# Kernel tuning notes

Hardware: AMD Instinct MI355X
Metric: run time of the kernel (lower is better)

Reference implementation:

```python
import jax, jax.numpy as jnp
import numpy as np

FWD_TRUNCATION = 0.05
EPS_LOG = 1e-20


def setup_inputs() -> dict:
    key = jax.random.key(0)
    k1, k2, k3, k4, k5 = jax.random.split(key, 5)
    B, N, M = 32768, 1024, 64
    samples = jax.random.normal(k1, (B, M), dtype=jnp.float32)
    mask = jax.random.uniform(k2, (B, M), dtype=jnp.float32)
    centroids = jax.random.normal(k3, (N, M), dtype=jnp.float32)
    # sd kept away from 0 to avoid huge 1/sd scaling
    sd = jax.random.uniform(k4, (1, M), dtype=jnp.float32) + 0.5
    log_marginal = jax.random.normal(k5, (1, N), dtype=jnp.float32)
    return {"samples": samples, "mask": mask, "centroids": centroids,
            "sd": sd, "log_marginal": log_marginal}


def _masked_pairwise_sq_distances(A, B, mask):
    # A: [B, M] samples, B: [N, M] centroids, mask: [B, M]
    sq_mask = mask * mask
    mA = mask * A
    A_d = jnp.sum(mA * mA, axis=1, keepdims=True)            # [B, 1]
    B_d = sq_mask @ (B * B).T                                 # [B, N]
    cross = (sq_mask * A) @ B.T                                # [B, N]
    return jax.nn.relu(A_d - 2.0 * cross + B_d)               # [B, N]


def _pdf_truncate(pdf, truncation):
    # discretePdfTruncate: zero out entries below truncation * rowmax, renormalize
    threshold = truncation * jnp.max(pdf, axis=-1, keepdims=True)
    pdf = jax.nn.relu(jnp.sign(pdf - threshold)) * pdf
    return pdf / jnp.sum(pdf, axis=-1, keepdims=True)


def reference(samples, mask, centroids, sd, log_marginal):
    # Mahalanobis: fold 1/sd into the mask (sqMahalanobisDistances)
    m = mask / sd
    dist = _masked_pairwise_sq_distances(samples, centroids, m)  # [B, N]
    log_prior = jax.nn.log_softmax(log_marginal, axis=-1)        # [1, N]
    logits = log_prior - 0.5 * dist                              # [B, N]
    # softmaxWithTemperature (temperature=1) -> truncate -> renormalize
    pdf = jax.nn.softmax(logits, axis=-1)
    pdf = _pdf_truncate(pdf, FWD_TRUNCATION)
    log_pdf = jnp.log(pdf + EPS_LOG)                             # logPdfTruncate
    return pdf, log_pdf
```

## Files before the change

kernel.cpp:

```cpp
#include <hip/hip_runtime.h>
#include <math.h>

#define N_C 1024
#define M_F 64
#define B_R 32768
#define R_B 32
#define LDX 132

typedef short bf16x8 __attribute__((ext_vector_type(8)));
typedef float f32x4 __attribute__((ext_vector_type(4)));
typedef unsigned int uint4v __attribute__((ext_vector_type(4)));

__device__ __forceinline__ short f2bf(float x) {
  unsigned b = __float_as_uint(x);
  b += 0x7fffu + ((b >> 16) & 1u);
  return (short)(b >> 16);
}
__device__ __forceinline__ float bf2f(short h) {
  return __uint_as_float(((unsigned)(unsigned short)h) << 16);
}

__device__ __forceinline__ void split3(const float* f, bf16x8& h, bf16x8& m, bf16x8& l) {
  uint4v hp, mp, lp;
#pragma unroll
  for (int i = 0; i < 4; ++i) {
    const unsigned b0 = __float_as_uint(f[2 * i]);
    const unsigned b1 = __float_as_uint(f[2 * i + 1]);
    const unsigned h0 = b0 & 0xFFFF0000u, h1 = b1 & 0xFFFF0000u;
    const float r0 = f[2 * i] - __uint_as_float(h0);
    const float r1 = f[2 * i + 1] - __uint_as_float(h1);
    hp[i] = (b0 >> 16) | h1;
    const unsigned rb0 = __float_as_uint(r0), rb1 = __float_as_uint(r1);
    const unsigned m0 = rb0 & 0xFFFF0000u, m1 = rb1 & 0xFFFF0000u;
    const float s0 = r0 - __uint_as_float(m0);
    const float s1 = r1 - __uint_as_float(m1);
    mp[i] = (rb0 >> 16) | m1;
    lp[i] = (__float_as_uint(s0) >> 16) | (__float_as_uint(s1) & 0xFFFF0000u);
  }
  h = __builtin_bit_cast(bf16x8, hp);
  m = __builtin_bit_cast(bf16x8, mp);
  l = __builtin_bit_cast(bf16x8, lp);
}

__global__ void prep(const float* __restrict__ centroids,
                     const float* __restrict__ lm,
                     bf16x8* __restrict__ yh, bf16x8* __restrict__ ym,
                     bf16x8* __restrict__ yl, float* __restrict__ lp) {
  __shared__ float red[256];
  const int t = threadIdx.x;

  if (blockIdx.x == 64) {
    float v[4];
    float mx = -INFINITY;
#pragma unroll
    for (int i = 0; i < 4; ++i) { v[i] = lm[i * 256 + t]; mx = fmaxf(mx, v[i]); }
    red[t] = mx;
    __syncthreads();
    for (int s = 128; s > 0; s >>= 1) {
      if (t < s) red[t] = fmaxf(red[t], red[t + s]);
      __syncthreads();
    }
    mx = red[0];
    __syncthreads();
    float sum = 0.f;
#pragma unroll
    for (int i = 0; i < 4; ++i) { v[i] -= mx; sum += expf(v[i]); }
    red[t] = sum;
    __syncthreads();
    for (int s = 128; s > 0; s >>= 1) {
      if (t < s) red[t] += red[t + s];
      __syncthreads();
    }
    const float l = logf(red[0]);
#pragma unroll
    for (int i = 0; i < 4; ++i) lp[i * 256 + t] = v[i] - l;
    return;
  }

  const int tid = blockIdx.x * 256 + t;
  const int l = tid & 63;
  const int c = (tid >> 6) & 63;
  const int s = tid >> 12;
  const int n = c * 16 + (l & 15);
  const int k0 = s * 32 + (l >> 4) * 8;
  bf16x8 h, mid, lo;
#pragma unroll
  for (int j = 0; j < 8; ++j) {
    const int k = k0 + j;
    float y;
    if (k < 64) {
      y = centroids[n * M_F + k];
    } else {
      const float cc = centroids[n * M_F + (k - 64)];
      y = cc * cc;
    }
    const short hh = f2bf(y);
    const float r1 = y - bf2f(hh);
    const short mm = f2bf(r1);
    const float r2 = r1 - bf2f(mm);
    h[j] = hh;
    mid[j] = mm;
    lo[j] = f2bf(r2);
  }
  const int blob = (s * 64 + c) * 64 + l;
  yh[blob] = h;
  ym[blob] = mid;
  yl[blob] = lo;
}

__global__ __launch_bounds__(256, 2) void rmm_main(
    const float* __restrict__ samples, const float* __restrict__ mask,
    const float* __restrict__ sd, const float* __restrict__ lp_g,
    const bf16x8* __restrict__ yh_g, const bf16x8* __restrict__ ym_g,
    const bf16x8* __restrict__ yl_g, float* __restrict__ out) {
  __shared__ float xs[R_B * LDX];
  __shared__ float lp_s[N_C];
  __shared__ float ad_s[R_B];
  __shared__ float red_s[R_B * 4];

  const int t = threadIdx.x;
  const int b0 = blockIdx.x * R_B;
  const int w = t >> 6;
  const int l = t & 63;
  const int m = l & 15;
  const int q = l >> 4;

  *(float4*)(lp_s + (t << 2)) = *(const float4*)(lp_g + (t << 2));

  const size_t base0 = (size_t)(w * 16) * 64 + l;
  bf16x8 Bh[2][2], Bm[2][2], Bl[2][2];
#pragma unroll
  for (int p = 0; p < 2; ++p)
#pragma unroll
    for (int e = 0; e < 2; ++e) {
      Bh[p][e] = yh_g[base0 + (p * 2 + e) * 64];
      Bm[p][e] = ym_g[base0 + (p * 2 + e) * 64];
      Bl[p][e] = yl_g[base0 + (p * 2 + e) * 64];
    }

  {
    const int r = t >> 3;
    const int j8 = (t & 7) << 3;
    const float* sp = samples + (size_t)(b0 + r) * M_F + j8;
    const float* mp = mask + (size_t)(b0 + r) * M_F + j8;
    float sa[8], ma[8], da[8];
    *(float4*)&sa[0] = *(const float4*)sp;
    *(float4*)&sa[4] = *(const float4*)(sp + 4);
    *(float4*)&ma[0] = *(const float4*)mp;
    *(float4*)&ma[4] = *(const float4*)(mp + 4);
    *(float4*)&da[0] = *(const float4*)(sd + j8);
    *(float4*)&da[4] = *(const float4*)(sd + j8 + 4);
    float ad = 0.f;
#pragma unroll
    for (int k = 0; k < 8; ++k) {
      const float mm = ma[k] / da[k];
      const float uu = mm * mm;
      const float mA = mm * sa[k];
      ad = fmaf(mA, mA, ad);
      xs[r * LDX + j8 + k] = -2.0f * (uu * sa[k]);
      xs[r * LDX + 64 + j8 + k] = uu;
    }
#pragma unroll
    for (int off = 1; off < 8; off <<= 1) ad += __shfl_xor(ad, off, 64);
    if ((t & 7) == 0) ad_s[r] = ad;
  }

  f32x4 acc[2][16];
#pragma unroll
  for (int mt = 0; mt < 2; ++mt)
#pragma unroll
    for (int c = 0; c < 16; ++c) acc[mt][c] = (f32x4){0.f, 0.f, 0.f, 0.f};

  __syncthreads();

  const int sx[8] = {1, 2, 0, 1, 2, 0, 1, 0};
  const int sy[8] = {2, 1, 2, 1, 0, 1, 0, 0};

#pragma unroll 1
  for (int s = 0; s < 4; ++s) {
    const size_t sbase = (size_t)(s * 64 + w * 16) * 64 + l;
    const bf16x8* yh = yh_g + sbase;
    const bf16x8* ym = ym_g + sbase;
    const bf16x8* yl = yl_g + sbase;

    bf16x8 A[3][2];
#pragma unroll
    for (int mt = 0; mt < 2; ++mt) {
      const float* xp = &xs[(mt * 16 + m) * LDX + s * 32 + q * 8];
      float av[8];
      *(float4*)&av[0] = *(const float4*)xp;
      *(float4*)&av[4] = *(const float4*)(xp + 4);
      split3(av, A[0][mt], A[1][mt], A[2][mt]);
    }

#pragma unroll
    for (int cp = 0; cp < 8; ++cp) {
      const int buf = cp & 1;
      const bf16x8 bh0 = Bh[buf][0], bm0 = Bm[buf][0], bl0 = Bl[buf][0];
      const bf16x8 bh1 = Bh[buf][1], bm1 = Bm[buf][1], bl1 = Bl[buf][1];
      const int pf0 = 2 * cp + 4;
      if (s < 3 || pf0 + 1 < 16) {
        const int o0 = (pf0 < 16) ? pf0 * 64 : 4096 + (pf0 - 16) * 64;
        const int o1 = (pf0 + 1 < 16) ? (pf0 + 1) * 64 : 4096 + (pf0 - 15) * 64;
        Bh[buf][0] = yh[o0]; Bm[buf][0] = ym[o0]; Bl[buf][0] = yl[o0];
        Bh[buf][1] = yh[o1]; Bm[buf][1] = ym[o1]; Bl[buf][1] = yl[o1];
      }
      const int c0 = 2 * cp, c1 = 2 * cp + 1;
#pragma unroll
      for (int sp = 0; sp < 8; ++sp) {
        const bf16x8 b0 = (sy[sp] == 0) ? bh0 : ((sy[sp] == 1) ? bm0 : bl0);
        const bf16x8 b1 = (sy[sp] == 0) ? bh1 : ((sy[sp] == 1) ? bm1 : bl1);
#pragma unroll
        for (int mt = 0; mt < 2; ++mt)
          acc[mt][c0] = __builtin_amdgcn_mfma_f32_16x16x32_bf16(
              A[sx[sp]][mt], b0, acc[mt][c0], 0, 0, 0);
#pragma unroll
        for (int mt = 0; mt < 2; ++mt)
          acc[mt][c1] = __builtin_amdgcn_mfma_f32_16x16x32_bf16(
              A[sx[sp]][mt], b1, acc[mt][c1], 0, 0, 0);
      }
    }
  }

  float adv[2][4];
#pragma unroll
  for (int mt = 0; mt < 2; ++mt)
#pragma unroll
    for (int g = 0; g < 4; ++g) adv[mt][g] = ad_s[mt * 16 + q * 4 + g];
  float lpv[16];
#pragma unroll
  for (int c = 0; c < 16; ++c) lpv[c] = lp_s[w * 256 + c * 16 + m];

#pragma unroll
  for (int mt = 0; mt < 2; ++mt)
#pragma unroll
    for (int c = 0; c < 16; ++c)
#pragma unroll
      for (int g = 0; g < 4; ++g) {
        const float dist = fmaxf(adv[mt][g] + acc[mt][c][g], 0.0f);
        acc[mt][c][g] = lpv[c] - 0.5f * dist;
      }

  float mx[2][4];
#pragma unroll
  for (int mt = 0; mt < 2; ++mt)
#pragma unroll
    for (int g = 0; g < 4; ++g) {
      float v = acc[mt][0][g];
#pragma unroll
      for (int c = 1; c < 16; ++c) v = fmaxf(v, acc[mt][c][g]);
#pragma unroll
      for (int off = 1; off < 16; off <<= 1) v = fmaxf(v, __shfl_xor(v, off, 64));
      mx[mt][g] = v;
    }
  if (m == 0) {
#pragma unroll
    for (int mt = 0; mt < 2; ++mt)
#pragma unroll
      for (int g = 0; g < 4; ++g) red_s[(mt * 16 + q * 4 + g) * 4 + w] = mx[mt][g];
  }
  __syncthreads();
#pragma unroll
  for (int mt = 0; mt < 2; ++mt)
#pragma unroll
    for (int g = 0; g < 4; ++g) {
      const float4 rv = *(const float4*)(&red_s[(mt * 16 + q * 4 + g) * 4]);
      mx[mt][g] = fmaxf(fmaxf(rv.x, rv.y), fmaxf(rv.z, rv.w));
    }
  __syncthreads();

  float sm[2][4];
#pragma unroll
  for (int mt = 0; mt < 2; ++mt)
#pragma unroll
    for (int g = 0; g < 4; ++g) {
      float ssum = 0.f;
#pragma unroll
      for (int c = 0; c < 16; ++c) {
        const float e = __expf(acc[mt][c][g] - mx[mt][g]);
        acc[mt][c][g] = e;
        ssum += e;
      }
#pragma unroll
      for (int off = 1; off < 16; off <<= 1) ssum += __shfl_xor(ssum, off, 64);
      sm[mt][g] = ssum;
    }
  if (m == 0) {
#pragma unroll
    for (int mt = 0; mt < 2; ++mt)
#pragma unroll
      for (int g = 0; g < 4; ++g) red_s[(mt * 16 + q * 4 + g) * 4 + w] = sm[mt][g];
  }
  __syncthreads();
#pragma unroll
  for (int mt = 0; mt < 2; ++mt)
#pragma unroll
    for (int g = 0; g < 4; ++g) {
      const float4 rv = *(const float4*)(&red_s[(mt * 16 + q * 4 + g) * 4]);
      sm[mt][g] = (rv.x + rv.y) + (rv.z + rv.w);
    }
  __syncthreads();

  float thr[2][4], qs[2][4];
#pragma unroll
  for (int mt = 0; mt < 2; ++mt)
#pragma unroll
    for (int g = 0; g < 4; ++g) {
      const float S1 = sm[mt][g];
      thr[mt][g] = 0.05f * (1.0f / S1);
      float s2 = 0.f;
#pragma unroll
      for (int c = 0; c < 16; ++c) {
        const float p = acc[mt][c][g] / S1;
        acc[mt][c][g] = p;
        s2 += (p > thr[mt][g]) ? p : 0.0f;
      }
#pragma unroll
      for (int off = 1; off < 16; off <<= 1) s2 += __shfl_xor(s2, off, 64);
      qs[mt][g] = s2;
    }
  if (m == 0) {
#pragma unroll
    for (int mt = 0; mt < 2; ++mt)
#pragma unroll
      for (int g = 0; g < 4; ++g) red_s[(mt * 16 + q * 4 + g) * 4 + w] = qs[mt][g];
  }
  __syncthreads();
#pragma unroll
  for (int mt = 0; mt < 2; ++mt)
#pragma unroll
    for (int g = 0; g < 4; ++g) {
      const float4 rv = *(const float4*)(&red_s[(mt * 16 + q * 4 + g) * 4]);
      qs[mt][g] = (rv.x + rv.y) + (rv.z + rv.w);
    }

  const size_t colbase = (size_t)(w * 256 + m);
#pragma unroll
  for (int mt = 0; mt < 2; ++mt)
#pragma unroll
    for (int g = 0; g < 4; ++g) {
      const float rq = 1.0f / qs[mt][g];
      float* orow = out + (size_t)(b0 + mt * 16 + q * 4 + g) * N_C + colbase;
      float* lrow = orow + (size_t)B_R * N_C;
#pragma unroll
      for (int c = 0; c < 16; ++c) {
        const float p = acc[mt][c][g];
        const float pf = (p > thr[mt][g]) ? (p * rq) : 0.0f;
        orow[c * 16] = pf;
        lrow[c * 16] = __logf(pf + 1e-20f);
      }
    }
}

extern "C" void kernel_launch(void* const* d_in, const int* in_sizes, int n_in,
                              void* d_out, int out_size, void* d_ws, size_t ws_size,
                              hipStream_t stream) {
  const float* samples   = (const float*)d_in[0];
  const float* mask      = (const float*)d_in[1];
  const float* centroids = (const float*)d_in[2];
  const float* sd        = (const float*)d_in[3];
  const float* lm        = (const float*)d_in[4];
  float* out = (float*)d_out;

  char* ws = (char*)d_ws;
  float* lp  = (float*)ws;
  bf16x8* yh = (bf16x8*)(ws + 4096);
  bf16x8* ym = (bf16x8*)(ws + 4096 + 262144);
  bf16x8* yl = (bf16x8*)(ws + 4096 + 2 * 262144);

  prep<<<65, 256, 0, stream>>>(centroids, lm, yh, ym, yl, lp);
  rmm_main<<<B_R / R_B, 256, 0, stream>>>(samples, mask, sd, lp, yh, ym, yl, out);
}
```

Measured before the change: 334.5 us.

## Process two row tiles per block with double-buffered sample staging

The grid is halved so each block handles two 32-row tiles. The second tile's sample/mask preprocessing is issued before the first tile's epilogue, and the B-fragment prefetch is refilled during that epilogue, so loads overlap compute. The log is also skipped for truncated entries, which now receive a precomputed log(1e-20) constant. This doubles the LDS used for the x buffers, which may lower occupancy, and leaves fewer blocks to spread across the CUs.

```diff
diff --git a/kernel.cpp b/kernel.cpp
--- a/kernel.cpp
+++ b/kernel.cpp
@@ -6,6 +6,7 @@
 #define B_R 32768
 #define R_B 32
 #define LDX 132
+#define NBLK 512
 
 typedef short bf16x8 __attribute__((ext_vector_type(8)));
 typedef float f32x4 __attribute__((ext_vector_type(4)));
@@ -108,74 +109,44 @@
   yl[blob] = lo;
 }
 
-__global__ __launch_bounds__(256, 2) void rmm_main(
-    const float* __restrict__ samples, const float* __restrict__ mask,
-    const float* __restrict__ sd, const float* __restrict__ lp_g,
-    const bf16x8* __restrict__ yh_g, const bf16x8* __restrict__ ym_g,
-    const bf16x8* __restrict__ yl_g, float* __restrict__ out) {
-  __shared__ float xs[R_B * LDX];
-  __shared__ float lp_s[N_C];
-  __shared__ float ad_s[R_B];
-  __shared__ float red_s[R_B * 4];
-
-  const int t = threadIdx.x;
-  const int b0 = blockIdx.x * R_B;
-  const int w = t >> 6;
-  const int l = t & 63;
-  const int m = l & 15;
-  const int q = l >> 4;
-
-  *(float4*)(lp_s + (t << 2)) = *(const float4*)(lp_g + (t << 2));
-
-  const size_t base0 = (size_t)(w * 16) * 64 + l;
-  bf16x8 Bh[2][2], Bm[2][2], Bl[2][2];
-#pragma unroll
-  for (int p = 0; p < 2; ++p)
-#pragma unroll
-    for (int e = 0; e < 2; ++e) {
-      Bh[p][e] = yh_g[base0 + (p * 2 + e) * 64];
-      Bm[p][e] = ym_g[base0 + (p * 2 + e) * 64];
-      Bl[p][e] = yl_g[base0 + (p * 2 + e) * 64];
-    }
-
-  {
-    const int r = t >> 3;
-    const int j8 = (t & 7) << 3;
-    const float* sp = samples + (size_t)(b0 + r) * M_F + j8;
-    const float* mp = mask + (size_t)(b0 + r) * M_F + j8;
-    float sa[8], ma[8], da[8];
-    *(float4*)&sa[0] = *(const float4*)sp;
-    *(float4*)&sa[4] = *(const float4*)(sp + 4);
-    *(float4*)&ma[0] = *(const float4*)mp;
-    *(float4*)&ma[4] = *(const float4*)(mp + 4);
-    *(float4*)&da[0] = *(const float4*)(sd + j8);
-    *(float4*)&da[4] = *(const float4*)(sd + j8 + 4);
-    float ad = 0.f;
-#pragma unroll
-    for (int k = 0; k < 8; ++k) {
-      const float mm = ma[k] / da[k];
-      const float uu = mm * mm;
-      const float mA = mm * sa[k];
-      ad = fmaf(mA, mA, ad);
-      xs[r * LDX + j8 + k] = -2.0f * (uu * sa[k]);
-      xs[r * LDX + 64 + j8 + k] = uu;
-    }
-#pragma unroll
-    for (int off = 1; off < 8; off <<= 1) ad += __shfl_xor(ad, off, 64);
-    if ((t & 7) == 0) ad_s[r] = ad;
-  }
-
-  f32x4 acc[2][16];
-#pragma unroll
-  for (int mt = 0; mt < 2; ++mt)
-#pragma unroll
-    for (int c = 0; c < 16; ++c) acc[mt][c] = (f32x4){0.f, 0.f, 0.f, 0.f};
-
-  __syncthreads();
-
+__device__ __forceinline__ void xbuild(const float* __restrict__ samples,
+                                       const float* __restrict__ mask,
+                                       const float* __restrict__ sd,
+                                       int b0, int t, float* xsb, float* adb) {
+  const int r = t >> 3;
+  const int j8 = (t & 7) << 3;
+  const float* sp = samples + (size_t)(b0 + r) * M_F + j8;
+  const float* mp = mask + (size_t)(b0 + r) * M_F + j8;
+  float sa[8], ma[8], da[8];
+  *(float4*)&sa[0] = *(const float4*)sp;
+  *(float4*)&sa[4] = *(const float4*)(sp + 4);
+  *(float4*)&ma[0] = *(const float4*)mp;
+  *(float4*)&ma[4] = *(const float4*)(mp + 4);
+  *(float4*)&da[0] = *(const float4*)(sd + j8);
+  *(float4*)&da[4] = *(const float4*)(sd + j8 + 4);
+  float ad = 0.f;
+#pragma unroll
+  for (int k = 0; k < 8; ++k) {
+    const float mm = ma[k] / da[k];
+    const float uu = mm * mm;
+    const float mA = mm * sa[k];
+    ad = fmaf(mA, mA, ad);
+    xsb[r * LDX + j8 + k] = -2.0f * (uu * sa[k]);
+    xsb[r * LDX + 64 + j8 + k] = uu;
+  }
+#pragma unroll
+  for (int off = 1; off < 8; off <<= 1) ad += __shfl_xor(ad, off, 64);
+  if ((t & 7) == 0) adb[r] = ad;
+}
+
+__device__ __forceinline__ void kloop(const bf16x8* __restrict__ yh_g,
+                                      const bf16x8* __restrict__ ym_g,
+                                      const bf16x8* __restrict__ yl_g,
+                                      const float* xsb, int w, int l, int m, int q,
+                                      bf16x8 (&Bh)[2][2], bf16x8 (&Bm)[2][2],
+                                      bf16x8 (&Bl)[2][2], f32x4 (&acc)[2][16]) {
   const int sx[8] = {1, 2, 0, 1, 2, 0, 1, 0};
   const int sy[8] = {2, 1, 2, 1, 0, 1, 0, 0};
-
 #pragma unroll 1
   for (int s = 0; s < 4; ++s) {
     const size_t sbase = (size_t)(s * 64 + w * 16) * 64 + l;
@@ -186,7 +157,7 @@
     bf16x8 A[3][2];
 #pragma unroll
     for (int mt = 0; mt < 2; ++mt) {
-      const float* xp = &xs[(mt * 16 + m) * LDX + s * 32 + q * 8];
+      const float* xp = &xsb[(mt * 16 + m) * LDX + s * 32 + q * 8];
       float av[8];
       *(float4*)&av[0] = *(const float4*)xp;
       *(float4*)&av[4] = *(const float4*)(xp + 4);
@@ -221,12 +192,21 @@
       }
     }
   }
-
+}
+
+template <int REFILL>
+__device__ __forceinline__ void epilogue(
+    f32x4 (&acc)[2][16], const float* adb, const float* lp_s, float* red_s,
+    int b0, int w, int l, int m, int q,
+    const bf16x8* __restrict__ yh_g, const bf16x8* __restrict__ ym_g,
+    const bf16x8* __restrict__ yl_g,
+    bf16x8 (&Bh)[2][2], bf16x8 (&Bm)[2][2], bf16x8 (&Bl)[2][2],
+    float* __restrict__ out) {
   float adv[2][4];
 #pragma unroll
   for (int mt = 0; mt < 2; ++mt)
 #pragma unroll
-    for (int g = 0; g < 4; ++g) adv[mt][g] = ad_s[mt * 16 + q * 4 + g];
+    for (int g = 0; g < 4; ++g) adv[mt][g] = adb[mt * 16 + q * 4 + g];
   float lpv[16];
 #pragma unroll
   for (int c = 0; c < 16; ++c) lpv[c] = lp_s[w * 256 + c * 16 + m];
@@ -325,6 +305,17 @@
 #pragma unroll
       for (int g = 0; g < 4; ++g) red_s[(mt * 16 + q * 4 + g) * 4 + w] = qs[mt][g];
   }
+  if constexpr (REFILL) {
+    const size_t base0 = (size_t)(w * 16) * 64 + l;
+#pragma unroll
+    for (int p = 0; p < 2; ++p)
+#pragma unroll
+      for (int e = 0; e < 2; ++e) {
+        Bh[p][e] = yh_g[base0 + (p * 2 + e) * 64];
+        Bm[p][e] = ym_g[base0 + (p * 2 + e) * 64];
+        Bl[p][e] = yl_g[base0 + (p * 2 + e) * 64];
+      }
+  }
   __syncthreads();
 #pragma unroll
   for (int mt = 0; mt < 2; ++mt)
@@ -333,6 +324,10 @@
       const float4 rv = *(const float4*)(&red_s[(mt * 16 + q * 4 + g) * 4]);
       qs[mt][g] = (rv.x + rv.y) + (rv.z + rv.w);
     }
+
+  float z20 = 1e-20f;
+  asm volatile("" : "+v"(z20));
+  const float L0 = __logf(z20);
 
   const size_t colbase = (size_t)(w * 256 + m);
 #pragma unroll
@@ -345,11 +340,73 @@
 #pragma unroll
       for (int c = 0; c < 16; ++c) {
         const float p = acc[mt][c][g];
-        const float pf = (p > thr[mt][g]) ? (p * rq) : 0.0f;
+        const bool keep = p > thr[mt][g];
+        const float pf = keep ? (p * rq) : 0.0f;
         orow[c * 16] = pf;
-        lrow[c * 16] = __logf(pf + 1e-20f);
-      }
-    }
+        lrow[c * 16] = keep ? __logf(pf + 1e-20f) : L0;
+      }
+    }
+}
+
+__global__ __launch_bounds__(256, 2) void rmm_main(
+    const float* __restrict__ samples, const float* __restrict__ mask,
+    const float* __restrict__ sd, const float* __restrict__ lp_g,
+    const bf16x8* __restrict__ yh_g, const bf16x8* __restrict__ ym_g,
+    const bf16x8* __restrict__ yl_g, float* __restrict__ out) {
+  __shared__ float xs[2][R_B * LDX];
+  __shared__ float lp_s[N_C];
+  __shared__ float ad_s[2][R_B];
+  __shared__ float red_s[R_B * 4];
+
+  const int t = threadIdx.x;
+  const int b0_0 = blockIdx.x * R_B;
+  const int b0_1 = (blockIdx.x + NBLK) * R_B;
+  const int w = t >> 6;
+  const int l = t & 63;
+  const int m = l & 15;
+  const int q = l >> 4;
+
+  *(float4*)(lp_s + (t << 2)) = *(const float4*)(lp_g + (t << 2));
+
+  const size_t base0 = (size_t)(w * 16) * 64 + l;
+  bf16x8 Bh[2][2], Bm[2][2], Bl[2][2];
+#pragma unroll
+  for (int p = 0; p < 2; ++p)
+#pragma unroll
+    for (int e = 0; e < 2; ++e) {
+      Bh[p][e] = yh_g[base0 + (p * 2 + e) * 64];
+      Bm[p][e] = ym_g[base0 + (p * 2 + e) * 64];
+      Bl[p][e] = yl_g[base0 + (p * 2 + e) * 64];
+    }
+
+  xbuild(samples, mask, sd, b0_0, t, &xs[0][0], &ad_s[0][0]);
+
+  f32x4 acc[2][16];
+#pragma unroll
+  for (int mt = 0; mt < 2; ++mt)
+#pragma unroll
+    for (int c = 0; c < 16; ++c) acc[mt][c] = (f32x4){0.f, 0.f, 0.f, 0.f};
+
+  __syncthreads();
+
+  kloop(yh_g, ym_g, yl_g, &xs[0][0], w, l, m, q, Bh, Bm, Bl, acc);
+
+  xbuild(samples, mask, sd, b0_1, t, &xs[1][0], &ad_s[1][0]);
+
+  epilogue<1>(acc, &ad_s[0][0], lp_s, red_s, b0_0, w, l, m, q,
+              yh_g, ym_g, yl_g, Bh, Bm, Bl, out);
+
+#pragma unroll
+  for (int mt = 0; mt < 2; ++mt)
+#pragma unroll
+    for (int c = 0; c < 16; ++c) acc[mt][c] = (f32x4){0.f, 0.f, 0.f, 0.f};
+
+  kloop(yh_g, ym_g, yl_g, &xs[1][0], w, l, m, q, Bh, Bm, Bl, acc);
+
+  __syncthreads();
+
+  epilogue<0>(acc, &ad_s[1][0], lp_s, red_s, b0_1, w, l, m, q,
+              yh_g, ym_g, yl_g, Bh, Bm, Bl, out);
 }
 
 extern "C" void kernel_launch(void* const* d_in, const int* in_sizes, int n_in,
@@ -369,5 +426,5 @@
   bf16x8* yl = (bf16x8*)(ws + 4096 + 2 * 262144);
 
   prep<<<65, 256, 0, stream>>>(centroids, lm, yh, ym, yl, lp);
-  rmm_main<<<B_R / R_B, 256, 0, stream>>>(samples, mask, sd, lp, yh, ym, yl, out);
-}
+  rmm_main<<<NBLK, 256, 0, stream>>>(samples, mask, sd, lp, yh, ym, yl, out);
+}
```

After: 360.3 us. +7.7%, slower.

## Double rows per block to 64 with 512 threads in two row halves

Applied to the files above, without the earlier changes.

Each block now handles 64 sample rows with 8 waves instead of 32 rows with 4 waves. The waves split into two row halves, and both halves use the same 4-wave column layout. All shared-memory indexing, the cross-wave reductions and the output rows gain an rh*32 offset. The aim is more centroid-fragment reuse per block (through cache) and more waves in flight. The cost is that launch_bounds(512,2) caps the register budget per wave, which risks spilling the 128-float accumulator. The grid is halved, and the larger per-block LDS footprint may limit residency.

```diff
diff --git a/kernel.cpp b/kernel.cpp
--- a/kernel.cpp
+++ b/kernel.cpp
@@ -4,7 +4,8 @@
 #define N_C 1024
 #define M_F 64
 #define B_R 32768
-#define R_B 32
+#define R_B 64
+#define NBLK (B_R / R_B)
 #define LDX 132
 
 typedef short bf16x8 __attribute__((ext_vector_type(8)));
@@ -108,7 +109,7 @@
   yl[blob] = lo;
 }
 
-__global__ __launch_bounds__(256, 2) void rmm_main(
+__global__ __launch_bounds__(512, 2) void rmm_main(
     const float* __restrict__ samples, const float* __restrict__ mask,
     const float* __restrict__ sd, const float* __restrict__ lp_g,
     const bf16x8* __restrict__ yh_g, const bf16x8* __restrict__ ym_g,
@@ -120,12 +121,14 @@
 
   const int t = threadIdx.x;
   const int b0 = blockIdx.x * R_B;
-  const int w = t >> 6;
+  const int wid = t >> 6;
+  const int w = wid & 3;
+  const int rh = wid >> 2;
   const int l = t & 63;
   const int m = l & 15;
   const int q = l >> 4;
 
-  *(float4*)(lp_s + (t << 2)) = *(const float4*)(lp_g + (t << 2));
+  if (t < 256) *(float4*)(lp_s + (t << 2)) = *(const float4*)(lp_g + (t << 2));
 
   const size_t base0 = (size_t)(w * 16) * 64 + l;
   bf16x8 Bh[2][2], Bm[2][2], Bl[2][2];
@@ -186,7 +189,7 @@
     bf16x8 A[3][2];
 #pragma unroll
     for (int mt = 0; mt < 2; ++mt) {
-      const float* xp = &xs[(mt * 16 + m) * LDX + s * 32 + q * 8];
+      const float* xp = &xs[(rh * 32 + mt * 16 + m) * LDX + s * 32 + q * 8];
       float av[8];
       *(float4*)&av[0] = *(const float4*)xp;
       *(float4*)&av[4] = *(const float4*)(xp + 4);
@@ -226,7 +229,7 @@
 #pragma unroll
   for (int mt = 0; mt < 2; ++mt)
 #pragma unroll
-    for (int g = 0; g < 4; ++g) adv[mt][g] = ad_s[mt * 16 + q * 4 + g];
+    for (int g = 0; g < 4; ++g) adv[mt][g] = ad_s[rh * 32 + mt * 16 + q * 4 + g];
   float lpv[16];
 #pragma unroll
   for (int c = 0; c < 16; ++c) lpv[c] = lp_s[w * 256 + c * 16 + m];
@@ -257,14 +260,15 @@
 #pragma unroll
     for (int mt = 0; mt < 2; ++mt)
 #pragma unroll
-      for (int g = 0; g < 4; ++g) red_s[(mt * 16 + q * 4 + g) * 4 + w] = mx[mt][g];
-  }
-  __syncthreads();
-#pragma unroll
-  for (int mt = 0; mt < 2; ++mt)
-#pragma unroll
-    for (int g = 0; g < 4; ++g) {
-      const float4 rv = *(const float4*)(&red_s[(mt * 16 + q * 4 + g) * 4]);
+      for (int g = 0; g < 4; ++g)
+        red_s[(rh * 32 + mt * 16 + q * 4 + g) * 4 + w] = mx[mt][g];
+  }
+  __syncthreads();
+#pragma unroll
+  for (int mt = 0; mt < 2; ++mt)
+#pragma unroll
+    for (int g = 0; g < 4; ++g) {
+      const float4 rv = *(const float4*)(&red_s[(rh * 32 + mt * 16 + q * 4 + g) * 4]);
       mx[mt][g] = fmaxf(fmaxf(rv.x, rv.y), fmaxf(rv.z, rv.w));
     }
   __syncthreads();
@@ -289,14 +293,15 @@
 #pragma unroll
     for (int mt = 0; mt < 2; ++mt)
 #pragma unroll
-      for (int g = 0; g < 4; ++g) red_s[(mt * 16 + q * 4 + g) * 4 + w] = sm[mt][g];
-  }
-  __syncthreads();
-#pragma unroll
-  for (int mt = 0; mt < 2; ++mt)
-#pragma unroll
-    for (int g = 0; g < 4; ++g) {
-      const float4 rv = *(const float4*)(&red_s[(mt * 16 + q * 4 + g) * 4]);
+      for (int g = 0; g < 4; ++g)
+        red_s[(rh * 32 + mt * 16 + q * 4 + g) * 4 + w] = sm[mt][g];
+  }
+  __syncthreads();
+#pragma unroll
+  for (int mt = 0; mt < 2; ++mt)
+#pragma unroll
+    for (int g = 0; g < 4; ++g) {
+      const float4 rv = *(const float4*)(&red_s[(rh * 32 + mt * 16 + q * 4 + g) * 4]);
       sm[mt][g] = (rv.x + rv.y) + (rv.z + rv.w);
     }
   __syncthreads();
@@ -323,14 +328,15 @@
 #pragma unroll
     for (int mt = 0; mt < 2; ++mt)
 #pragma unroll
-      for (int g = 0; g < 4; ++g) red_s[(mt * 16 + q * 4 + g) * 4 + w] = qs[mt][g];
-  }
-  __syncthreads();
-#pragma unroll
-  for (int mt = 0; mt < 2; ++mt)
-#pragma unroll
-    for (int g = 0; g < 4; ++g) {
-      const float4 rv = *(const float4*)(&red_s[(mt * 16 + q * 4 + g) * 4]);
+      for (int g = 0; g < 4; ++g)
+        red_s[(rh * 32 + mt * 16 + q * 4 + g) * 4 + w] = qs[mt][g];
+  }
+  __syncthreads();
+#pragma unroll
+  for (int mt = 0; mt < 2; ++mt)
+#pragma unroll
+    for (int g = 0; g < 4; ++g) {
+      const float4 rv = *(const float4*)(&red_s[(rh * 32 + mt * 16 + q * 4 + g) * 4]);
       qs[mt][g] = (rv.x + rv.y) + (rv.z + rv.w);
     }
 
@@ -340,7 +346,7 @@
 #pragma unroll
     for (int g = 0; g < 4; ++g) {
       const float rq = 1.0f / qs[mt][g];
-      float* orow = out + (size_t)(b0 + mt * 16 + q * 4 + g) * N_C + colbase;
+      float* orow = out + (size_t)(b0 + rh * 32 + mt * 16 + q * 4 + g) * N_C + colbase;
       float* lrow = orow + (size_t)B_R * N_C;
 #pragma unroll
       for (int c = 0; c < 16; ++c) {
@@ -369,5 +375,5 @@
   bf16x8* yl = (bf16x8*)(ws + 4096 + 2 * 262144);
 
   prep<<<65, 256, 0, stream>>>(centroids, lm, yh, ym, yl, lp);
-  rmm_main<<<B_R / R_B, 256, 0, stream>>>(samples, mask, sd, lp, yh, ym, yl, out);
-}
+  rmm_main<<<NBLK, 512, 0, stream>>>(samples, mask, sd, lp, yh, ym, yl, out);
+}
```

Measured after the change: 355.3 us. +6.2%, slower.
